# Performance work log

Measured on AMD Instinct MI355X. Metric: run time of the kernel, lower is better.

Reference implementation:

```python
import jax, jax.numpy as jnp
import numpy as np

N = 4096          # number of agents
TOP_K = 12        # config.TOP_K
OBS_RADIUS = 1.0  # config.OBS_RADIUS


def setup_inputs() -> dict:
    key = jax.random.key(0)
    ks = jax.random.split(key, 10)

    def lin(k, o, i):
        return jax.random.normal(k, (o, i), dtype=jnp.float32) * (1.0 / np.sqrt(i))

    x = jax.random.normal(ks[0], (N, N, 4), dtype=jnp.float32)
    r = jnp.asarray(0.25, dtype=jnp.float32)  # safety radius subtracted from d_norm
    W1 = lin(ks[1], 64, 6);   b1 = jax.random.normal(ks[2], (64,), jnp.float32) * 0.01
    W2 = lin(ks[3], 128, 64); b2 = jax.random.normal(ks[4], (128,), jnp.float32) * 0.01
    W3 = lin(ks[5], 64, 128); b3 = jax.random.normal(ks[6], (64,), jnp.float32) * 0.01
    W4 = lin(ks[7], 1, 64);   b4 = jax.random.normal(ks[8], (1,), jnp.float32) * 0.01
    return {"x": x, "r": r, "W1": W1, "b1": b1, "W2": W2, "b2": b2,
            "W3": W3, "b3": b3, "W4": W4, "b4": b4}


def reference(x, r, W1, b1, W2, b2, W3, b3, W4, b4):
    n = x.shape[0]
    # d_norm with eps added INSIDE the sum (matches torch: sum(x**2 + 1e-4))
    d_norm = jnp.sqrt(jnp.sum(x[:, :, :2] ** 2 + 0.0001, axis=2, keepdims=True))  # [n,n,1]
    eye = jnp.eye(n, dtype=x.dtype)[:, :, None]                                   # [n,n,1]
    xf = jnp.concatenate([x, eye, d_norm - r], axis=2)                            # [n,n,6]

    # remove_distant_agents: top-k nearest by 2D norm (eps 1e-6 inside sum)
    dn = jnp.sqrt(jnp.sum(xf[:, :, :2] ** 2 + 1e-06, axis=2))                     # [n,n]
    _, idx = jax.lax.top_k(-dn, TOP_K)                                            # [n,K]
    xg = jnp.take_along_axis(xf, idx[:, :, None], axis=1)                         # [n,K,6]

    dist = jnp.sqrt(jnp.sum(xg[:, :, :2] ** 2 + 0.0001, axis=2, keepdims=True))   # [n,K,1]
    mask = (dist <= OBS_RADIUS).astype(xg.dtype)

    # 1x1 Conv1d stack == per-neighbor MLP
    h = jax.nn.relu(jnp.einsum('nkc,oc->nko', xg, W1) + b1)
    h = jax.nn.relu(jnp.einsum('nkc,oc->nko', h, W2) + b2)
    h = jax.nn.relu(jnp.einsum('nkc,oc->nko', h, W3) + b3)
    out = (jnp.einsum('nkc,oc->nko', h, W4) + b4) * mask                          # [n,K,1]

    rows = jnp.broadcast_to(jnp.arange(n)[:, None], (n, TOP_K))
    indices = jnp.stack([rows, idx], axis=2).reshape(-1, 2)                       # [n*K,2]
    return out, mask, indices
```

## Files before the change

kernel.cpp:

```cpp
#include <hip/hip_runtime.h>

#define NN    4096
#define TOPK  12
#define NP    (NN * TOPK)
#define OFF_MASK (NP)
#define OFF_IDX  (2 * NP)

__global__ __launch_bounds__(256, 6) void topk_rows(const float* __restrict__ x,
                                                    float* __restrict__ out) {
    const int i    = blockIdx.x;
    const int t    = threadIdx.x;
    const int lane = t & 63;
    const int w    = t >> 6;
    const float4* x4 = (const float4*)x + (size_t)i * NN;

    float s[16];
    #pragma unroll
    for (int k = 0; k < 16; ++k) {
        float4 v = x4[(k << 8) + t];
        s[k] = v.x * v.x + v.y * v.y;
    }

    unsigned long long bk;
    {
        float bs = s[0]; int bj = t;
        #pragma unroll
        for (int k = 1; k < 16; ++k) {
            int j = (k << 8) + t;
            if (s[k] < bs) { bs = s[k]; bj = j; }
        }
        bk = ((unsigned long long)__float_as_uint(bs) << 32) | (unsigned)bj;
    }

    __shared__ unsigned long long cand[4 * TOPK];

    unsigned long long mykey = ~0ULL;

    for (int it = 0; it < TOPK; ++it) {
        unsigned long long vk = bk;
        #pragma unroll
        for (int off = 1; off < 64; off <<= 1) {
            unsigned long long ok = __shfl_xor(vk, off, 64);
            vk = (ok < vk) ? ok : vk;
        }
        if (lane == it) mykey = vk;
        int wj = (int)(vk & 0xffffffffULL);
        if ((wj & 63) == lane) {
            int kk = wj >> 8;
            #pragma unroll
            for (int k = 0; k < 16; ++k)
                if (k == kk) s[k] = 3.0e38f;
            float bs = s[0]; int bj = t;
            #pragma unroll
            for (int k = 1; k < 16; ++k) {
                int j = (k << 8) + t;
                if (s[k] < bs) { bs = s[k]; bj = j; }
            }
            bk = ((unsigned long long)__float_as_uint(bs) << 32) | (unsigned)bj;
        }
    }

    if (lane < TOPK) cand[w * TOPK + lane] = mykey;
    __syncthreads();

    if (w == 0) {
        unsigned long long key = (lane < 4 * TOPK) ? cand[lane] : ~0ULL;
        #pragma unroll
        for (int k = 2; k <= 64; k <<= 1) {
            #pragma unroll
            for (int jj = k >> 1; jj >= 1; jj >>= 1) {
                unsigned long long ok = __shfl_xor(key, jj, 64);
                bool keepMin = ((lane & k) == 0) == ((lane & jj) == 0);
                unsigned long long mn = (ok < key) ? ok : key;
                unsigned long long mx = (ok < key) ? key : ok;
                key = keepMin ? mn : mx;
            }
        }
        if (lane < TOPK) {
            int   j  = (int)(key & 0xffffffffULL);
            float ss = __uint_as_float((unsigned)(key >> 32));
            float d  = sqrtf(ss + 2.0e-4f);
            float mask = (d <= 1.0f) ? 1.0f : 0.0f;
            int p = i * TOPK + lane;
            out[OFF_MASK + p]        = mask;
            out[OFF_IDX + 2 * p]     = (float)i;
            out[OFF_IDX + 2 * p + 1] = (float)j;
        }
    }
}

__global__ __launch_bounds__(512, 6) void mlp_block(
        const float* __restrict__ x, const float* __restrict__ rp,
        const float* __restrict__ W1, const float* __restrict__ b1,
        const float* __restrict__ W2, const float* __restrict__ b2,
        const float* __restrict__ W3, const float* __restrict__ b3,
        const float* __restrict__ W4, const float* __restrict__ b4,
        float* out) {
    __shared__ float h1s[64 * 64];
    __shared__ float h2s[128 * 64];
    __shared__ float p4s[8 * 64];

    const int t  = threadIdx.x;
    const int pl = t & 63;
    const int ch = __builtin_amdgcn_readfirstlane(t >> 6);
    const int p  = blockIdx.x * 64 + pl;
    const int i  = p / TOPK;
    const int j  = (int)out[OFF_IDX + 2 * p + 1];

    const float4 v = ((const float4*)x)[(size_t)i * NN + j];
    const float d  = sqrtf(v.x * v.x + v.y * v.y + 2.0e-4f);
    float xin[6];
    xin[0] = v.x; xin[1] = v.y; xin[2] = v.z; xin[3] = v.w;
    xin[4] = (i == j) ? 1.0f : 0.0f;
    xin[5] = d - rp[0];

    #pragma unroll
    for (int q = 0; q < 8; ++q) {
        int m = ch * 8 + q;
        const float* w = W1 + m * 6;
        float a = b1[m];
        #pragma unroll
        for (int c = 0; c < 6; ++c) a += w[c] * xin[c];
        h1s[m * 64 + pl] = fmaxf(a, 0.0f);
    }
    __syncthreads();

    float acc[16];
    #pragma unroll
    for (int q = 0; q < 16; ++q) acc[q] = b2[ch * 16 + q];
    for (int part = 0; part < 4; ++part) {
        float h1r[16];
        #pragma unroll
        for (int k = 0; k < 16; ++k) h1r[k] = h1s[(part * 16 + k) * 64 + pl];
        #pragma unroll
        for (int q = 0; q < 16; ++q) {
            const float* w = W2 + (ch * 16 + q) * 64 + part * 16;
            #pragma unroll
            for (int k = 0; k < 16; ++k) acc[q] += w[k] * h1r[k];
        }
    }
    #pragma unroll
    for (int q = 0; q < 16; ++q) h2s[(ch * 16 + q) * 64 + pl] = fmaxf(acc[q], 0.0f);
    __syncthreads();

    float h3[8];
    #pragma unroll
    for (int q = 0; q < 8; ++q) h3[q] = b3[ch * 8 + q];
    for (int part = 0; part < 8; ++part) {
        float h2r[16];
        #pragma unroll
        for (int k = 0; k < 16; ++k) h2r[k] = h2s[(part * 16 + k) * 64 + pl];
        #pragma unroll
        for (int q = 0; q < 8; ++q) {
            const float* w = W3 + (ch * 8 + q) * 128 + part * 16;
            #pragma unroll
            for (int k = 0; k < 16; ++k) h3[q] += w[k] * h2r[k];
        }
    }
    float partial = 0.0f;
    #pragma unroll
    for (int q = 0; q < 8; ++q) partial += W4[ch * 8 + q] * fmaxf(h3[q], 0.0f);
    p4s[ch * 64 + pl] = partial;
    __syncthreads();

    if (t < 64) {
        float s = b4[0];
        #pragma unroll
        for (int c = 0; c < 8; ++c) s += p4s[c * 64 + t];
        int pp = blockIdx.x * 64 + t;
        out[pp] = s * out[OFF_MASK + pp];
    }
}

extern "C" void kernel_launch(void* const* d_in, const int* in_sizes, int n_in,
                              void* d_out, int out_size, void* d_ws, size_t ws_size,
                              hipStream_t stream) {
    const float* x  = (const float*)d_in[0];
    const float* rp = (const float*)d_in[1];
    const float* W1 = (const float*)d_in[2];
    const float* b1 = (const float*)d_in[3];
    const float* W2 = (const float*)d_in[4];
    const float* b2 = (const float*)d_in[5];
    const float* W3 = (const float*)d_in[6];
    const float* b3 = (const float*)d_in[7];
    const float* W4 = (const float*)d_in[8];
    const float* b4 = (const float*)d_in[9];
    float* out = (float*)d_out;

    topk_rows<<<NN, 256, 0, stream>>>(x, out);
    mlp_block<<<NP / 64, 512, 0, stream>>>(x, rp, W1, b1, W2, b2, W3, b3, W4, b4, out);
}
```

Measured before the change: 412.5 us.

## Fuse top-k selection and per-neighbor MLP into one kernel with four rows per block

New measurement: 580.8 us. +40.8%, slower.

```diff
diff --git a/kernel.cpp b/kernel.cpp
--- a/kernel.cpp
+++ b/kernel.cpp
@@ -5,37 +5,48 @@
 #define NP    (NN * TOPK)
 #define OFF_MASK (NP)
 #define OFF_IDX  (2 * NP)
+#define RPB   4
+#define NPAIR (RPB * TOPK)
 
-__global__ __launch_bounds__(256, 6) void topk_rows(const float* __restrict__ x,
-                                                    float* __restrict__ out) {
-    const int i    = blockIdx.x;
+__global__ __launch_bounds__(1024, 8) void fused_cbf(
+        const float* __restrict__ x, const float* __restrict__ rp,
+        const float* __restrict__ W1, const float* __restrict__ b1,
+        const float* __restrict__ W2, const float* __restrict__ b2,
+        const float* __restrict__ W3, const float* __restrict__ b3,
+        const float* __restrict__ W4, const float* __restrict__ b4,
+        float* __restrict__ out) {
+    __shared__ unsigned long long cand[RPB][NPAIR];
+    __shared__ int   selj[RPB][TOPK];
+    __shared__ float seld[RPB][TOPK];
+    __shared__ float h1s[64 * NPAIR];
+    __shared__ float h2s[128 * NPAIR];
+    __shared__ float p4s[16 * NPAIR];
+
     const int t    = threadIdx.x;
+    const int r    = t >> 8;
+    const int tt   = t & 255;
     const int lane = t & 63;
-    const int w    = t >> 6;
+    const int wrow = tt >> 6;
+    const int i    = blockIdx.x * RPB + r;
     const float4* x4 = (const float4*)x + (size_t)i * NN;
 
     float s[16];
     #pragma unroll
     for (int k = 0; k < 16; ++k) {
-        float4 v = x4[(k << 8) + t];
+        float4 v = x4[(k << 8) + tt];
         s[k] = v.x * v.x + v.y * v.y;
     }
-
     unsigned long long bk;
     {
-        float bs = s[0]; int bj = t;
+        float bs = s[0]; int bj = tt;
         #pragma unroll
         for (int k = 1; k < 16; ++k) {
-            int j = (k << 8) + t;
+            int j = (k << 8) + tt;
             if (s[k] < bs) { bs = s[k]; bj = j; }
         }
         bk = ((unsigned long long)__float_as_uint(bs) << 32) | (unsigned)bj;
     }
-
-    __shared__ unsigned long long cand[4 * TOPK];
-
     unsigned long long mykey = ~0ULL;
-
     for (int it = 0; it < TOPK; ++it) {
         unsigned long long vk = bk;
         #pragma unroll
@@ -50,125 +61,120 @@
             #pragma unroll
             for (int k = 0; k < 16; ++k)
                 if (k == kk) s[k] = 3.0e38f;
-            float bs = s[0]; int bj = t;
+            float bs = s[0]; int bj = tt;
             #pragma unroll
             for (int k = 1; k < 16; ++k) {
-                int j = (k << 8) + t;
+                int j = (k << 8) + tt;
                 if (s[k] < bs) { bs = s[k]; bj = j; }
             }
             bk = ((unsigned long long)__float_as_uint(bs) << 32) | (unsigned)bj;
         }
     }
-
-    if (lane < TOPK) cand[w * TOPK + lane] = mykey;
+    if (lane < TOPK) cand[r][wrow * TOPK + lane] = mykey;
     __syncthreads();
 
-    if (w == 0) {
-        unsigned long long key = (lane < 4 * TOPK) ? cand[lane] : ~0ULL;
-        #pragma unroll
-        for (int k = 2; k <= 64; k <<= 1) {
+    {
+        const int W = t >> 6;
+        if (W < RPB) {
+            unsigned long long key = (lane < NPAIR) ? cand[W][lane] : ~0ULL;
             #pragma unroll
-            for (int jj = k >> 1; jj >= 1; jj >>= 1) {
-                unsigned long long ok = __shfl_xor(key, jj, 64);
-                bool keepMin = ((lane & k) == 0) == ((lane & jj) == 0);
-                unsigned long long mn = (ok < key) ? ok : key;
-                unsigned long long mx = (ok < key) ? key : ok;
-                key = keepMin ? mn : mx;
+            for (int k = 2; k <= 64; k <<= 1) {
+                #pragma unroll
+                for (int jj = k >> 1; jj >= 1; jj >>= 1) {
+                    unsigned long long ok = __shfl_xor(key, jj, 64);
+                    bool keepMin = ((lane & k) == 0) == ((lane & jj) == 0);
+                    unsigned long long mn = (ok < key) ? ok : key;
+                    unsigned long long mx = (ok < key) ? key : ok;
+                    key = keepMin ? mn : mx;
+                }
+            }
+            if (lane < TOPK) {
+                int   j  = (int)(key & 0xffffffffULL);
+                float ss = __uint_as_float((unsigned)(key >> 32));
+                float d  = sqrtf(ss + 2.0e-4f);
+                int ii = blockIdx.x * RPB + W;
+                int p  = ii * TOPK + lane;
+                out[OFF_MASK + p]        = (d <= 1.0f) ? 1.0f : 0.0f;
+                out[OFF_IDX + 2 * p]     = (float)ii;
+                out[OFF_IDX + 2 * p + 1] = (float)j;
+                selj[W][lane] = j;
+                seld[W][lane] = d;
             }
         }
-        if (lane < TOPK) {
-            int   j  = (int)(key & 0xffffffffULL);
-            float ss = __uint_as_float((unsigned)(key >> 32));
-            float d  = sqrtf(ss + 2.0e-4f);
-            float mask = (d <= 1.0f) ? 1.0f : 0.0f;
-            int p = i * TOPK + lane;
-            out[OFF_MASK + p]        = mask;
-            out[OFF_IDX + 2 * p]     = (float)i;
-            out[OFF_IDX + 2 * p + 1] = (float)j;
-        }
     }
-}
+    __syncthreads();
 
-__global__ __launch_bounds__(512, 6) void mlp_block(
-        const float* __restrict__ x, const float* __restrict__ rp,
-        const float* __restrict__ W1, const float* __restrict__ b1,
-        const float* __restrict__ W2, const float* __restrict__ b2,
-        const float* __restrict__ W3, const float* __restrict__ b3,
-        const float* __restrict__ W4, const float* __restrict__ b4,
-        float* out) {
-    __shared__ float h1s[64 * 64];
-    __shared__ float h2s[128 * 64];
-    __shared__ float p4s[8 * 64];
-
-    const int t  = threadIdx.x;
-    const int pl = t & 63;
-    const int ch = __builtin_amdgcn_readfirstlane(t >> 6);
-    const int p  = blockIdx.x * 64 + pl;
-    const int i  = p / TOPK;
-    const int j  = (int)out[OFF_IDX + 2 * p + 1];
-
-    const float4 v = ((const float4*)x)[(size_t)i * NN + j];
-    const float d  = sqrtf(v.x * v.x + v.y * v.y + 2.0e-4f);
+    const int  pl     = lane;
+    const bool active = (pl < NPAIR);
+    const int  ch     = __builtin_amdgcn_readfirstlane(t >> 6);
+    const int  pls    = active ? pl : 0;
+    const int  pr     = pls / TOPK;
+    const int  pk     = pls % TOPK;
+    const int  jn     = selj[pr][pk];
+    const float d     = seld[pr][pk];
+    const int  ii     = blockIdx.x * RPB + pr;
+    const float4 v = ((const float4*)x)[(size_t)ii * NN + jn];
     float xin[6];
     xin[0] = v.x; xin[1] = v.y; xin[2] = v.z; xin[3] = v.w;
-    xin[4] = (i == j) ? 1.0f : 0.0f;
+    xin[4] = (ii == jn) ? 1.0f : 0.0f;
     xin[5] = d - rp[0];
 
     #pragma unroll
-    for (int q = 0; q < 8; ++q) {
-        int m = ch * 8 + q;
+    for (int q = 0; q < 4; ++q) {
+        int m = ch * 4 + q;
         const float* w = W1 + m * 6;
         float a = b1[m];
         #pragma unroll
         for (int c = 0; c < 6; ++c) a += w[c] * xin[c];
-        h1s[m * 64 + pl] = fmaxf(a, 0.0f);
+        if (active) h1s[m * NPAIR + pl] = fmaxf(a, 0.0f);
     }
     __syncthreads();
 
-    float acc[16];
+    float acc[8];
     #pragma unroll
-    for (int q = 0; q < 16; ++q) acc[q] = b2[ch * 16 + q];
+    for (int q = 0; q < 8; ++q) acc[q] = b2[ch * 8 + q];
     for (int part = 0; part < 4; ++part) {
         float h1r[16];
         #pragma unroll
-        for (int k = 0; k < 16; ++k) h1r[k] = h1s[(part * 16 + k) * 64 + pl];
+        for (int k = 0; k < 16; ++k) h1r[k] = h1s[(part * 16 + k) * NPAIR + pls];
         #pragma unroll
-        for (int q = 0; q < 16; ++q) {
-            const float* w = W2 + (ch * 16 + q) * 64 + part * 16;
+        for (int q = 0; q < 8; ++q) {
+            const float* w = W2 + (ch * 8 + q) * 64 + part * 16;
             #pragma unroll
             for (int k = 0; k < 16; ++k) acc[q] += w[k] * h1r[k];
         }
     }
     #pragma unroll
-    for (int q = 0; q < 16; ++q) h2s[(ch * 16 + q) * 64 + pl] = fmaxf(acc[q], 0.0f);
+    for (int q = 0; q < 8; ++q)
+        if (active) h2s[(ch * 8 + q) * NPAIR + pl] = fmaxf(acc[q], 0.0f);
     __syncthreads();
 
-    float h3[8];
+    float h3[4];
     #pragma unroll
-    for (int q = 0; q < 8; ++q) h3[q] = b3[ch * 8 + q];
+    for (int q = 0; q < 4; ++q) h3[q] = b3[ch * 4 + q];
     for (int part = 0; part < 8; ++part) {
         float h2r[16];
         #pragma unroll
-        for (int k = 0; k < 16; ++k) h2r[k] = h2s[(part * 16 + k) * 64 + pl];
+        for (int k = 0; k < 16; ++k) h2r[k] = h2s[(part * 16 + k) * NPAIR + pls];
         #pragma unroll
-        for (int q = 0; q < 8; ++q) {
-            const float* w = W3 + (ch * 8 + q) * 128 + part * 16;
+        for (int q = 0; q < 4; ++q) {
+            const float* w = W3 + (ch * 4 + q) * 128 + part * 16;
             #pragma unroll
             for (int k = 0; k < 16; ++k) h3[q] += w[k] * h2r[k];
         }
     }
     float partial = 0.0f;
     #pragma unroll
-    for (int q = 0; q < 8; ++q) partial += W4[ch * 8 + q] * fmaxf(h3[q], 0.0f);
-    p4s[ch * 64 + pl] = partial;
+    for (int q = 0; q < 4; ++q) partial += W4[ch * 4 + q] * fmaxf(h3[q], 0.0f);
+    if (active) p4s[ch * NPAIR + pl] = partial;
     __syncthreads();
 
-    if (t < 64) {
-        float s = b4[0];
+    if (t < NPAIR) {
+        float sum = b4[0];
         #pragma unroll
-        for (int c = 0; c < 8; ++c) s += p4s[c * 64 + t];
-        int pp = blockIdx.x * 64 + t;
-        out[pp] = s * out[OFF_MASK + pp];
+        for (int c = 0; c < 16; ++c) sum += p4s[c * NPAIR + t];
+        float dd = seld[t / TOPK][t % TOPK];
+        out[blockIdx.x * NPAIR + t] = sum * ((dd <= 1.0f) ? 1.0f : 0.0f);
     }
 }
 
@@ -187,6 +193,6 @@
     const float* b4 = (const float*)d_in[9];
     float* out = (float*)d_out;
 
-    topk_rows<<<NN, 256, 0, stream>>>(x, out);
-    mlp_block<<<NP / 64, 512, 0, stream>>>(x, rp, W1, b1, W2, b2, W3, b3, W4, b4, out);
+    fused_cbf<<<NN / RPB, 1024, 0, stream>>>(x, rp, W1, b1, W2, b2,
+                                             W3, b3, W4, b4, out);
 }
```
